# Kernel tuning notes

Hardware: AMD Instinct MI355X
Metric: run time of the kernel (lower is better)

Reference implementation:

```python
import jax, jax.numpy as jnp
import numpy as np

IN_F = 4096
OUT_F = 4096
GROUP = 128                      # quantization group size
NG = IN_F * OUT_F // GROUP       # 131072 groups
LORA_R = 16
LORA_SCALE = 32.0 / 16.0         # lora_alpha / lora_r


def _dequant(indices, codebook, scales):
    # Unpack two INT4 nibbles per byte: low nibble first, then high (interleaved).
    low = indices & 15
    high = (indices >> 4) & 15
    idx = jnp.stack([low, high], axis=1).reshape(-1)          # [numel]
    # Codebook lookup, per-group scaling.
    vals = codebook[idx].reshape(NG, GROUP) * scales[:, None]  # [NG, GROUP]
    return vals.reshape(OUT_F, IN_F)


def setup_inputs() -> dict:
    key = jax.random.key(0)
    ks = jax.random.split(key, 7)
    return {
        "x": jax.random.normal(ks[0], (4, 2048, IN_F), dtype=jnp.float32),
        "indices": jax.random.randint(ks[1], (IN_F * OUT_F // 2,), 0, 256, dtype=jnp.int32),
        "codebook": jax.random.normal(ks[2], (16,), dtype=jnp.float32),
        "scales": jax.random.uniform(ks[3], (NG,), dtype=jnp.float32, minval=0.01, maxval=1.0),
        "lora_A": jax.random.normal(ks[4], (IN_F, LORA_R), dtype=jnp.float32) / 64.0,
        "lora_B": jax.random.normal(ks[5], (LORA_R, OUT_F), dtype=jnp.float32) / 64.0,
        "bias": jax.random.normal(ks[6], (OUT_F,), dtype=jnp.float32),
    }


def reference(x, indices, codebook, scales, lora_A, lora_B, bias):
    # lowram path: dequantize INT4 codebook weights, F.linear, fused LoRA add, bias.
    W = _dequant(indices, codebook, scales)                    # [OUT_F, IN_F]
    h = jnp.einsum('bsi,oi->bso', x, W)                        # F.linear (no bias yet)
    h = h + (x @ lora_A) @ lora_B * LORA_SCALE                 # LoRA adapter (dropout=0)
    return h + bias
```

## Files before the change

### kernel.cpp

```cpp
#include <hip/hip_runtime.h>
#include <stdint.h>

#define IN_F   4096
#define OUT_F  4096
#define M_TOT  8192
#define KDIM   4096

typedef float          f32x4  __attribute__((ext_vector_type(4)));
typedef int            i32x4  __attribute__((ext_vector_type(4)));
typedef unsigned short u16x8  __attribute__((ext_vector_type(8)));
typedef __bf16         bf16x8 __attribute__((ext_vector_type(8)));

__device__ __forceinline__ unsigned short f2bf(float f) {
  uint32_t u = __builtin_bit_cast(uint32_t, f);
  u = (u + 0x7FFFu + ((u >> 16) & 1u)) >> 16;
  return (unsigned short)u;
}
__device__ __forceinline__ float bf2f(unsigned short s) {
  return __builtin_bit_cast(float, (uint32_t)s << 16);
}

__device__ __forceinline__ void gld_lds16(const void* g, void* l) {
  __builtin_amdgcn_global_load_lds((const __attribute__((address_space(1))) void*)g,
                                   (__attribute__((address_space(3))) void*)l,
                                   16, 0, 0);
}

__global__ __launch_bounds__(256) void k_xcast(const f32x4* __restrict__ x,
                                               u16x8* __restrict__ xb) {
  int t = blockIdx.x * 256 + threadIdx.x;
  f32x4 a = x[2 * t];
  f32x4 b = x[2 * t + 1];
  u16x8 o;
  o[0] = f2bf(a[0]); o[1] = f2bf(a[1]); o[2] = f2bf(a[2]); o[3] = f2bf(a[3]);
  o[4] = f2bf(b[0]); o[5] = f2bf(b[1]); o[6] = f2bf(b[2]); o[7] = f2bf(b[3]);
  xb[t] = o;
}

__global__ __launch_bounds__(256) void k_lora(const float* __restrict__ A,
                                              const float* __restrict__ Bm,
                                              unsigned short* __restrict__ L) {
  __shared__ float sB[16][64];
  const int ib = blockIdx.x * 256;
  const int ob = blockIdx.y * 64;
  const int t  = threadIdx.x;
  for (int j = 0; j < 4; ++j) {
    int idx = t + j * 256;
    int r = idx >> 6, oc = idx & 63;
    sB[r][oc] = Bm[r * OUT_F + ob + oc];
  }
  float a[16];
  const f32x4* Ap = (const f32x4*)(A + (size_t)(ib + t) * 16);
  #pragma unroll
  for (int j = 0; j < 4; ++j) {
    f32x4 v = Ap[j];
    a[4*j+0] = v[0]; a[4*j+1] = v[1]; a[4*j+2] = v[2]; a[4*j+3] = v[3];
  }
  __syncthreads();
  unsigned short* Lp = L + (size_t)ob * IN_F + ib + t;
  #pragma unroll 4
  for (int oc = 0; oc < 64; ++oc) {
    float acc = 0.f;
    #pragma unroll
    for (int r = 0; r < 16; ++r) acc += a[r] * sB[r][oc];
    Lp[(size_t)oc * IN_F] = f2bf(acc * 2.0f);
  }
}

__global__ __launch_bounds__(256) void k_dequant(const int* __restrict__ idx,
                                                 const float* __restrict__ cb,
                                                 const float* __restrict__ scales,
                                                 const unsigned short* __restrict__ L,
                                                 unsigned short* __restrict__ Wc) {
  __shared__ float scb[16];
  const int t = blockIdx.x * 256 + threadIdx.x;
  if (threadIdx.x < 16) scb[threadIdx.x] = cb[threadIdx.x];
  __syncthreads();
  i32x4 w = ((const i32x4*)idx)[t];
  float sc = scales[t >> 4];
  u16x8 lw = ((const u16x8*)L)[t];
  u16x8 o;
  #pragma unroll
  for (int j = 0; j < 4; ++j) {
    int word = w[j];
    float v0 = scb[word & 15] * sc + bf2f(lw[2 * j]);
    float v1 = scb[(word >> 4) & 15] * sc + bf2f(lw[2 * j + 1]);
    o[2 * j]     = f2bf(v0);
    o[2 * j + 1] = f2bf(v1);
  }
  ((u16x8*)Wc)[t] = o;
}


#define BARR()  __builtin_amdgcn_s_barrier()
#define LGKM0() asm volatile("s_waitcnt lgkmcnt(0)" ::: "memory")
#define VMC0()  asm volatile("s_waitcnt vmcnt(0)" ::: "memory")

#define STAGE_A(kt, ha, c) do {                                                          \
  gld_lds16(Ag + (size_t)((ha) * 128) * KDIM + (kt) * 64,                                \
            smem + (c) * 32768 + (ha) * 16384 + ldsw);                                   \
  gld_lds16(Ag + (size_t)((ha) * 128 + 64) * KDIM + (kt) * 64,                           \
            smem + (c) * 32768 + (ha) * 16384 + 8192 + ldsw);                            \
} while (0)

#define STAGE_B(kt, hb, c) do {                                                          \
  gld_lds16(Bg + (size_t)((hb) * 128) * KDIM + (kt) * 64,                                \
            smem + 65536 + (c) * 32768 + (hb) * 16384 + ldsw);                           \
  gld_lds16(Bg + (size_t)((hb) * 128 + 64) * KDIM + (kt) * 64,                           \
            smem + 65536 + (c) * 32768 + (hb) * 16384 + 8192 + ldsw);                    \
} while (0)

#define READ_B4(DST, c, COFF) do {                                                       \
  const char* _p = smem + 65536 + (c) * 32768 + rowB;                                    \
  _Pragma("unroll")                                                                      \
  for (int n = 0; n < 4; ++n)                                                            \
    DST[n] = *(const bf16x8*)(_p + n * 2048 + (COFF));                                   \
} while (0)

#define READ_A8(DST, c, COFF) do {                                                       \
  const char* _p = smem + (c) * 32768 + rowA;                                            \
  _Pragma("unroll")                                                                      \
  for (int m16 = 0; m16 < 8; ++m16)                                                      \
    DST[m16] = *(const bf16x8*)(_p + m16 * 2048 + (COFF));                               \
} while (0)

#define MFMA32(AF, BF) do {                                                              \
  __builtin_amdgcn_s_setprio(1);                                                         \
  _Pragma("unroll")                                                                      \
  for (int m16 = 0; m16 < 8; ++m16)                                                      \
    _Pragma("unroll")                                                                    \
    for (int n = 0; n < 4; ++n)                                                          \
      acc[m16][n] = __builtin_amdgcn_mfma_f32_16x16x32_bf16(AF[m16], BF[n],              \
                                                            acc[m16][n], 0, 0, 0);      \
  __builtin_amdgcn_s_setprio(0);                                                         \
} while (0)

#define TILE5(t_, c_, doStage) do {                                                      \
  if (doStage) {                                                                         \
    STAGE_B((t_) + 1, 0, (c_) ^ 1); STAGE_B((t_) + 1, 1, (c_) ^ 1);                      \
    STAGE_A((t_) + 1, 0, (c_) ^ 1); STAGE_A((t_) + 1, 1, (c_) ^ 1);                      \
  }                                                                                      \
  READ_B4(bfrX, c_, coffX); READ_A8(afX, c_, coffX);                                     \
  MFMA32(afX, bfrX);                                                                     \
  READ_B4(bfrY, c_, coffY); READ_A8(afY, c_, coffY);                                     \
  MFMA32(afY, bfrY);                                                                     \
  LGKM0(); VMC0(); BARR();                                                               \
} while (0)

__global__ __launch_bounds__(512, 2) void k_gemm(const unsigned short* __restrict__ A,
                                                 const unsigned short* __restrict__ B,
                                                 const float* __restrict__ bias,
                                                 float* __restrict__ C) {
  __shared__ char smem[131072];
  const int tid  = threadIdx.x;
  const int lane = tid & 63;
  const int wv   = tid >> 6;
  const int wm   = wv >> 2;
  const int wn   = wv & 3;
  const int r    = lane & 15;
  const int q    = lane >> 4;
  const int xr   = r & 7;
  const int coff0 = (q ^ xr) << 4;
  const int coff1 = ((q + 4) ^ xr) << 4;
  const int coffX = (wv & 1) ? coff1 : coff0;
  const int coffY = (wv & 1) ? coff0 : coff1;
  const int rowA = (wm * 128 + r) * 128;
  const int rowB = (wn * 64 + r) * 128;
  const int srow = tid >> 3;
  const int scol = ((tid & 7) ^ ((tid >> 3) & 7)) * 8;
  const int ldsw = wv * 1024;
  const int bm = blockIdx.x;
  const int bn = blockIdx.y;

  const unsigned short* Ag = A + (size_t)(bm * 256 + srow) * KDIM + scol;
  const unsigned short* Bg = B + (size_t)(bn * 256 + srow) * KDIM + scol;

  bf16x8 afX[8], afY[8], bfrX[4], bfrY[4];
  f32x4 acc[8][4];
  #pragma unroll
  for (int m = 0; m < 8; ++m)
    #pragma unroll
    for (int n = 0; n < 4; ++n)
      acc[m][n] = (f32x4){0.f, 0.f, 0.f, 0.f};

  STAGE_B(0, 0, 0); STAGE_B(0, 1, 0); STAGE_A(0, 0, 0); STAGE_A(0, 1, 0);
  VMC0();
  BARR();

  #pragma unroll 1
  for (int t = 0; t < 62; t += 2) {
    TILE5(t,     0, 1);
    TILE5(t + 1, 1, 1);
  }
  TILE5(62, 0, 1);
  TILE5(63, 1, 0);

  __syncthreads();
  {
    char* eps = smem + wv * 4096;
    const int row0 = bm * 256 + wm * 128;
    const int col0 = bn * 256 + wn * 64;
    const f32x4 bias4 = *(const f32x4*)(bias + col0 + r * 4);
    #pragma unroll
    for (int mi = 0; mi < 8; ++mi) {
      #pragma unroll
      for (int j = 0; j < 4; ++j)
        #pragma unroll
        for (int ni = 0; ni < 4; ++ni)
          *(float*)(eps + (((q * 4 + j) * 64) + ni * 16 + r) * 4) = acc[mi][ni][j];
      LGKM0();
      __builtin_amdgcn_sched_barrier(0);
      #pragma unroll
      for (int p = 0; p < 4; ++p) {
        const int row = p * 4 + q;
        f32x4 v = *(const f32x4*)(eps + row * 256 + r * 16);
        v[0] += bias4[0]; v[1] += bias4[1]; v[2] += bias4[2]; v[3] += bias4[3];
        *(f32x4*)(C + (size_t)(row0 + mi * 16 + row) * OUT_F + col0 + r * 4) = v;
      }
      asm volatile("" ::: "memory");
    }
  }
}

extern "C" void kernel_launch(void* const* d_in, const int* in_sizes, int n_in,
                              void* d_out, int out_size, void* d_ws, size_t ws_size,
                              hipStream_t stream) {
  const float* x    = (const float*)d_in[0];
  const int*   idx  = (const int*)d_in[1];
  const float* cb   = (const float*)d_in[2];
  const float* scl  = (const float*)d_in[3];
  const float* lA   = (const float*)d_in[4];
  const float* lB   = (const float*)d_in[5];
  const float* bias = (const float*)d_in[6];
  float* out = (float*)d_out;

  unsigned short* xb = (unsigned short*)d_ws;
  unsigned short* Wc = (unsigned short*)((char*)d_ws + (size_t)M_TOT * KDIM * 2);
  unsigned short* Lbuf = (unsigned short*)d_out;

  k_xcast<<<16384, 256, 0, stream>>>((const f32x4*)x, (u16x8*)xb);
  k_lora<<<dim3(16, 64), 256, 0, stream>>>(lA, lB, Lbuf);
  k_dequant<<<8192, 256, 0, stream>>>(idx, cb, scl, Lbuf, Wc);
  k_gemm<<<dim3(32, 16), 512, 0, stream>>>(xb, Wc, bias, out);
}
```

Before: 280.3 us.

## Make each GEMM block compute two N tiles, prefetching the second during the first epilogue

Halves the GEMM grid so each workgroup computes two 256-column output tiles in sequence. The first K-stage of the second tile is loaded while the last tile of the first pass is computed, and the first epilogue writes through a different LDS region so the loads can overlap it. This removes some launch and prologue cost and hides pipeline fill behind the epilogue. In exchange the grid drops to 256 blocks (2 per CU at 512 threads), which may leave some compute units less occupied and lengthens each block.

```diff
diff --git a/kernel.cpp b/kernel.cpp
--- a/kernel.cpp
+++ b/kernel.cpp
@@ -104,9 +104,9 @@
 } while (0)
 
 #define STAGE_B(kt, hb, c) do {                                                          \
-  gld_lds16(Bg + (size_t)((hb) * 128) * KDIM + (kt) * 64,                                \
+  gld_lds16(Bgv + (size_t)((hb) * 128) * KDIM + (kt) * 64,                               \
             smem + 65536 + (c) * 32768 + (hb) * 16384 + ldsw);                           \
-  gld_lds16(Bg + (size_t)((hb) * 128 + 64) * KDIM + (kt) * 64,                           \
+  gld_lds16(Bgv + (size_t)((hb) * 128 + 64) * KDIM + (kt) * 64,                          \
             smem + 65536 + (c) * 32768 + (hb) * 16384 + 8192 + ldsw);                    \
 } while (0)
 
@@ -145,6 +145,39 @@
   READ_B4(bfrY, c_, coffY); READ_A8(afY, c_, coffY);                                     \
   MFMA32(afY, bfrY);                                                                     \
   LGKM0(); VMC0(); BARR();                                                               \
+} while (0)
+
+#define EPI(EPSOFF, COL0) do {                                                           \
+  char* eps = smem + (EPSOFF) + wv * 4096;               \
+  const int row0e = bm * 256 + wm * 128;                                                 \
+  const int col0e = (COL0) + wn * 64;                                                    \
+  const f32x4 bias4 = *(const f32x4*)(bias + col0e + r * 4);                             \
+  _Pragma("unroll")                                                                      \
+  for (int mi = 0; mi < 8; ++mi) {                                                       \
+    _Pragma("unroll")                                                                    \
+    for (int j = 0; j < 4; ++j)                                                          \
+      _Pragma("unroll")                                                                  \
+      for (int ni = 0; ni < 4; ++ni)                                                     \
+        *(float*)(eps + (((q * 4 + j) * 64) + ni * 16 + r) * 4) = acc[mi][ni][j];        \
+    LGKM0();                                                                             \
+    __builtin_amdgcn_sched_barrier(0);                                                   \
+    _Pragma("unroll")                                                                    \
+    for (int p = 0; p < 4; ++p) {                                                        \
+      const int row = p * 4 + q;                                                         \
+      f32x4 v = *(const f32x4*)(eps + row * 256 + r * 16);                               \
+      v[0] += bias4[0]; v[1] += bias4[1]; v[2] += bias4[2]; v[3] += bias4[3];            \
+      *(f32x4*)(C + (size_t)(row0e + mi * 16 + row) * OUT_F + col0e + r * 4) = v;        \
+    }                                                                                    \
+    asm volatile("" ::: "memory");                  \
+  }                                                                                      \
+} while (0)
+
+#define ZERO_ACC() do {                                                                  \
+  _Pragma("unroll")                                                                      \
+  for (int m = 0; m < 8; ++m)                                                            \
+    _Pragma("unroll")                                                                    \
+    for (int n = 0; n < 4; ++n)                                                          \
+      acc[m][n] = (f32x4){0.f, 0.f, 0.f, 0.f};                                           \
 } while (0)
 
 __global__ __launch_bounds__(512, 2) void k_gemm(const unsigned short* __restrict__ A,
@@ -169,19 +202,17 @@
   const int srow = tid >> 3;
   const int scol = ((tid & 7) ^ ((tid >> 3) & 7)) * 8;
   const int ldsw = wv * 1024;
-  const int bm = blockIdx.x;
-  const int bn = blockIdx.y;
-
-  const unsigned short* Ag = A + (size_t)(bm * 256 + srow) * KDIM + scol;
-  const unsigned short* Bg = B + (size_t)(bn * 256 + srow) * KDIM + scol;
+  const int bm  = blockIdx.x;
+  const int bn0 = blockIdx.y;
+
+  const unsigned short* Ag  = A + (size_t)(bm * 256 + srow) * KDIM + scol;
+  const unsigned short* Bg0 = B + (size_t)(bn0 * 256 + srow) * KDIM + scol;
+  const unsigned short* Bg1 = Bg0 + (size_t)(8 * 256) * KDIM;
+  const unsigned short* Bgv = Bg0;
 
   bf16x8 afX[8], afY[8], bfrX[4], bfrY[4];
   f32x4 acc[8][4];
-  #pragma unroll
-  for (int m = 0; m < 8; ++m)
-    #pragma unroll
-    for (int n = 0; n < 4; ++n)
-      acc[m][n] = (f32x4){0.f, 0.f, 0.f, 0.f};
+  ZERO_ACC();
 
   STAGE_B(0, 0, 0); STAGE_B(0, 1, 0); STAGE_A(0, 0, 0); STAGE_A(0, 1, 0);
   VMC0();
@@ -193,33 +224,29 @@
     TILE5(t + 1, 1, 1);
   }
   TILE5(62, 0, 1);
+
+  Bgv = Bg1;
+  STAGE_B(0, 0, 0); STAGE_B(0, 1, 0); STAGE_A(0, 0, 0); STAGE_A(0, 1, 0);
+  READ_B4(bfrX, 1, coffX); READ_A8(afX, 1, coffX);
+  MFMA32(afX, bfrX);
+  READ_B4(bfrY, 1, coffY); READ_A8(afY, 1, coffY);
+  MFMA32(afY, bfrY);
+  __syncthreads();
+
+  EPI(32768, bn0 * 256);
+  __syncthreads();
+  ZERO_ACC();
+
+  #pragma unroll 1
+  for (int t = 0; t < 62; t += 2) {
+    TILE5(t,     0, 1);
+    TILE5(t + 1, 1, 1);
+  }
+  TILE5(62, 0, 1);
   TILE5(63, 1, 0);
 
   __syncthreads();
-  {
-    char* eps = smem + wv * 4096;
-    const int row0 = bm * 256 + wm * 128;
-    const int col0 = bn * 256 + wn * 64;
-    const f32x4 bias4 = *(const f32x4*)(bias + col0 + r * 4);
-    #pragma unroll
-    for (int mi = 0; mi < 8; ++mi) {
-      #pragma unroll
-      for (int j = 0; j < 4; ++j)
-        #pragma unroll
-        for (int ni = 0; ni < 4; ++ni)
-          *(float*)(eps + (((q * 4 + j) * 64) + ni * 16 + r) * 4) = acc[mi][ni][j];
-      LGKM0();
-      __builtin_amdgcn_sched_barrier(0);
-      #pragma unroll
-      for (int p = 0; p < 4; ++p) {
-        const int row = p * 4 + q;
-        f32x4 v = *(const f32x4*)(eps + row * 256 + r * 16);
-        v[0] += bias4[0]; v[1] += bias4[1]; v[2] += bias4[2]; v[3] += bias4[3];
-        *(f32x4*)(C + (size_t)(row0 + mi * 16 + row) * OUT_F + col0 + r * 4) = v;
-      }
-      asm volatile("" ::: "memory");
-    }
-  }
+  EPI(0, (bn0 + 8) * 256);
 }
 
 extern "C" void kernel_launch(void* const* d_in, const int* in_sizes, int n_in,
@@ -241,5 +268,5 @@
   k_xcast<<<16384, 256, 0, stream>>>((const f32x4*)x, (u16x8*)xb);
   k_lora<<<dim3(16, 64), 256, 0, stream>>>(lA, lB, Lbuf);
   k_dequant<<<8192, 256, 0, stream>>>(idx, cb, scl, Lbuf, Wc);
-  k_gemm<<<dim3(32, 16), 512, 0, stream>>>(xb, Wc, bias, out);
-}
+  k_gemm<<<dim3(32, 8), 512, 0, stream>>>(xb, Wc, bias, out);
+}
```

Result: slower. 294.6 us (+5.1%).
